# Kernel optimization log

Measured on AMD Instinct MI355X. Metric: run time of the kernel, lower is better.

## Reference

```python
import jax, jax.numpy as jnp
import numpy as np

ALPHA = 4.0   # spikingjelly surrogate.Sigmoid default
TAU = 2.0
VTH = 1.0
EPS = 1e-5

@jax.custom_vjp
def spike(x):
    return (x >= 0.0).astype(x.dtype)

def _spike_fwd(x):
    return spike(x), x

def _spike_bwd(x, g):
    s = jax.nn.sigmoid(ALPHA * x)
    return (g * ALPHA * s * (1.0 - s),)

spike.defvjp(_spike_fwd, _spike_bwd)

def lif(x):
    # x: [T, B, N, C]; multi-step LIF, v_reset=0 hard reset, detach_reset=True
    def step(v, xt):
        v = v + (xt - v) / TAU          # charge
        s = spike(v - VTH)              # fire (surrogate grad)
        v = v * (1.0 - jax.lax.stop_gradient(s))  # hard reset, detached
        return v, s
    _, out = jax.lax.scan(step, jnp.zeros_like(x[0]), x)
    return out

def bn(x, gamma, beta):
    # BatchNorm1d in training mode: per-channel (last dim) over all other dims
    mu = x.mean(axis=(0, 1, 2), keepdims=True)
    var = x.var(axis=(0, 1, 2), keepdims=True)  # biased var, as torch BN uses for normalization
    return (x - mu) * jax.lax.rsqrt(var + EPS) * gamma + beta

def setup_inputs() -> dict:
    key = jax.random.key(0)
    ks = jax.random.split(key, 3)
    T, B, N, C, H = 4, 32, 1024, 256, 256
    x = jax.random.normal(ks[0], (T, B, N, C), dtype=jnp.float32)
    W1 = jax.random.normal(ks[1], (C, H), dtype=jnp.float32) * (1.0 / np.sqrt(C))
    W2 = jax.random.normal(ks[2], (H, C), dtype=jnp.float32) * (1.0 / np.sqrt(H))
    return {
        "x": x,
        "W1": W1, "b1": jnp.zeros((H,), jnp.float32),
        "gamma1": jnp.ones((H,), jnp.float32), "beta1": jnp.zeros((H,), jnp.float32),
        "W2": W2, "b2": jnp.zeros((C,), jnp.float32),
        "gamma2": jnp.ones((C,), jnp.float32), "beta2": jnp.zeros((C,), jnp.float32),
    }

def reference(x, W1, b1, gamma1, beta1, W2, b2, gamma2, beta2):
    # fc1: Linear -> BN (per-channel over T*B*N) -> multi-step LIF
    h = jnp.einsum('tbnc,ch->tbnh', x, W1) + b1
    h = lif(bn(h, gamma1, beta1))
    # fc2
    o = jnp.einsum('tbnh,ho->tbno', h, W2) + b2
    return lif(bn(o, gamma2, beta2))
```

## Files before the change

kernel.cpp:

```cpp
#include <hip/hip_runtime.h>


typedef __attribute__((ext_vector_type(8))) short bf16x8;
typedef __attribute__((ext_vector_type(8))) _Float16 f16x8;
typedef __attribute__((ext_vector_type(4))) _Float16 f16x4;
typedef __attribute__((ext_vector_type(4))) float f32x4;

__device__ __forceinline__ unsigned short f32_to_bf16_rne(float f) {
    unsigned int u = __builtin_bit_cast(unsigned int, f);
    u += 0x7FFFu + ((u >> 16) & 1u);
    return (unsigned short)(u >> 16);
}
__device__ __forceinline__ float bf16_to_f32(unsigned short h) {
    unsigned int u = ((unsigned int)h) << 16;
    return __builtin_bit_cast(float, u);
}
__device__ __forceinline__ int xcd_swz(int bid, int nwg) {
    int per = nwg >> 3;
    return (bid & 7) * per + (bid >> 3);
}

__global__ __launch_bounds__(256) void split_w1(const float* __restrict__ W1,
                                                _Float16* __restrict__ BhiT,
                                                _Float16* __restrict__ BloT) {
    int i = blockIdx.x * 256 + threadIdx.x;
    int k = i >> 8, n = i & 255;
    float w = W1[i];
    _Float16 hi = (_Float16)w;
    _Float16 lo = (_Float16)((w - (float)hi) * 4096.0f);
    BhiT[(size_t)n * 256 + k] = hi;
    BloT[(size_t)n * 256 + k] = lo;
}

__global__ __launch_bounds__(256) void split_w2(const float* __restrict__ W2,
                                                unsigned short* __restrict__ Bt) {
    int i = blockIdx.x * 256 + threadIdx.x;
    int k = i >> 8, n = i & 255;
    float w = W2[i];
    unsigned short hi = f32_to_bf16_rne(w);
    float r = w - bf16_to_f32(hi);
    unsigned short mid = f32_to_bf16_rne(r);
    float r2 = r - bf16_to_f32(mid);
    unsigned short lo = f32_to_bf16_rne(r2);
    Bt[(size_t)(0 * 256 + n) * 256 + k] = hi;
    Bt[(size_t)(1 * 256 + n) * 256 + k] = mid;
    Bt[(size_t)(2 * 256 + n) * 256 + k] = lo;
}

__global__ __launch_bounds__(512, 4) void gemm1_mfma(const float* __restrict__ A,
                                                     const _Float16* __restrict__ Bhi,
                                                     const _Float16* __restrict__ Blo,
                                                     const float* __restrict__ bias,
                                                     float* __restrict__ C,
                                                     double* __restrict__ partial) {
    __shared__ __align__(16) _Float16 Ahi[64 * 256];
    __shared__ __align__(16) _Float16 Alo[64 * 256];
    const int blk = xcd_swz(blockIdx.x, gridDim.x);
    const size_t m0 = (size_t)blk * 64;
    const int tid = threadIdx.x;
    const int lane = tid & 63;
    const int wave = tid >> 6;
    const int lrow = lane & 15, lchunk = lane >> 4;

    const _Float16* BhiB = Bhi + ((size_t)(32 * wave + lrow)) * 256 + lchunk * 8;
    const _Float16* BloB = Blo + ((size_t)(32 * wave + lrow)) * 256 + lchunk * 8;

    {
        const float* src = A + m0 * 256;
        float4 rr[8];
#pragma unroll
        for (int it = 0; it < 8; ++it)
            rr[it] = *(const float4*)(src + (size_t)(it * 512 + tid) * 4);
#pragma unroll
        for (int it = 0; it < 8; ++it) {
            unsigned i4 = (unsigned)(it * 512 + tid);
            float f[4] = {rr[it].x, rr[it].y, rr[it].z, rr[it].w};
            f16x4 hi4, lo4;
#pragma unroll
            for (int e = 0; e < 4; ++e) {
                _Float16 hh = (_Float16)f[e];
                hi4[e] = hh;
                lo4[e] = (_Float16)((f[e] - (float)hh) * 4096.0f);
            }
            unsigned off = i4 * 8u;
            unsigned swz = off ^ (((off >> 9) & 7u) << 4);
            *(f16x4*)((char*)Ahi + swz) = hi4;
            *(f16x4*)((char*)Alo + swz) = lo4;
        }
    }
    __syncthreads();

    f32x4 acc0[4][2] = {}, acc1[4][2] = {};

#pragma unroll
    for (int k0 = 0; k0 < 8; ++k0) {
        f16x8 bh[2], bl[2];
#pragma unroll
        for (int nf = 0; nf < 2; ++nf) {
            bh[nf] = *(const f16x8*)(BhiB + nf * 4096 + k0 * 32);
            bl[nf] = *(const f16x8*)(BloB + nf * 4096 + k0 * 32);
        }
#pragma unroll
        for (int half = 0; half < 2; ++half) {
            f16x8 ah[2], al[2];
#pragma unroll
            for (int m = 0; m < 2; ++m) {
                unsigned r = (unsigned)(32 * half + 16 * m + lrow);
                unsigned off = (r * 512u + (unsigned)(k0 * 64 + lchunk * 16)) ^ ((r & 7u) << 4);
                ah[m] = *(const f16x8*)((const char*)Ahi + off);
                al[m] = *(const f16x8*)((const char*)Alo + off);
            }
            __builtin_amdgcn_s_setprio(1);
#pragma unroll
            for (int nf = 0; nf < 2; ++nf)
#pragma unroll
                for (int m = 0; m < 2; ++m) {
                    const int mf = half * 2 + m;
                    acc0[mf][nf] = __builtin_amdgcn_mfma_f32_16x16x32_f16(
                        ah[m], bh[nf], acc0[mf][nf], 0, 0, 0);
                    acc1[mf][nf] = __builtin_amdgcn_mfma_f32_16x16x32_f16(
                        ah[m], bl[nf], acc1[mf][nf], 0, 0, 0);
                    acc1[mf][nf] = __builtin_amdgcn_mfma_f32_16x16x32_f16(
                        al[m], bh[nf], acc1[mf][nf], 0, 0, 0);
                }
            __builtin_amdgcn_s_setprio(0);
        }
    }

    const float UNSCALE = 1.0f / 4096.0f;
#pragma unroll
    for (int nf = 0; nf < 2; ++nf) {
        int col = 32 * wave + 16 * nf + lrow;
        float bvv = bias[col];
        double ss = 0.0, qq = 0.0;
#pragma unroll
        for (int mf = 0; mf < 4; ++mf) {
            size_t rowb = m0 + 16 * mf + 4 * lchunk;
#pragma unroll
            for (int e = 0; e < 4; ++e) {
                float hv = acc0[mf][nf][e] + acc1[mf][nf][e] * UNSCALE + bvv;
                C[(rowb + e) * 256 + col] = hv;
                ss += (double)hv;
                qq += (double)hv * (double)hv;
            }
        }
        ss += __shfl_xor(ss, 16);
        ss += __shfl_xor(ss, 32);
        qq += __shfl_xor(qq, 16);
        qq += __shfl_xor(qq, 32);
        if (lane < 16) {
            partial[(size_t)blk * 512 + col] = ss;
            partial[(size_t)blk * 512 + 256 + col] = qq;
        }
    }
}

__global__ __launch_bounds__(512, 4) void gemm2_fused(const float* __restrict__ h,
                                                      const float2* __restrict__ ss1,
                                                      const unsigned short* __restrict__ Bt,
                                                      const float* __restrict__ bias,
                                                      float* __restrict__ C,
                                                      double* __restrict__ partial,
                                                      int bnRows) {
    __shared__ __align__(16) unsigned short Asw[64 * 256];
    const int blk = xcd_swz(blockIdx.x, gridDim.x);
    const int bn0 = blk * 16;
    const int tid = threadIdx.x;
    const int lane = tid & 63;
    const int wave = tid >> 6;
    const int lrow = lane & 15, lchunk = lane >> 4;

    const unsigned short* Bbase =
        Bt + ((size_t)(32 * wave + lrow)) * 256 + lchunk * 8;

    {
        float4 rr[8];
#pragma unroll
        for (int it = 0; it < 2; ++it) {
            int slot = it * 512 + tid;
            int bn = slot >> 6;
            int colq = slot & 63;
            size_t rb = (size_t)(bn0 + bn) * 256 + colq * 4;
#pragma unroll
            for (int t4 = 0; t4 < 4; ++t4)
                rr[it * 4 + t4] = *(const float4*)(h + (size_t)t4 * bnRows * 256 + rb);
        }
#pragma unroll
        for (int it = 0; it < 2; ++it) {
            int slot = it * 512 + tid;
            int bn = slot >> 6;
            int colq = slot & 63;
            int c0 = colq * 4;
            float2 p0 = ss1[c0], p1 = ss1[c0 + 1], p2 = ss1[c0 + 2], p3 = ss1[c0 + 3];
            float4 v = make_float4(0.f, 0.f, 0.f, 0.f);
#pragma unroll
            for (int t4 = 0; t4 < 4; ++t4) {
                float4 hv = rr[it * 4 + t4];
                float x0 = hv.x * p0.x + p0.y;
                float x1 = hv.y * p1.x + p1.y;
                float x2 = hv.z * p2.x + p2.y;
                float x3 = hv.w * p3.x + p3.y;
                v.x = (v.x + x0) * 0.5f;
                v.y = (v.y + x1) * 0.5f;
                v.z = (v.z + x2) * 0.5f;
                v.w = (v.w + x3) * 0.5f;
                ushort4 sp;
                sp.x = (v.x >= 1.0f) ? 0x3F80 : 0;
                sp.y = (v.y >= 1.0f) ? 0x3F80 : 0;
                sp.z = (v.z >= 1.0f) ? 0x3F80 : 0;
                sp.w = (v.w >= 1.0f) ? 0x3F80 : 0;
                v.x = (v.x >= 1.0f) ? 0.0f : v.x;
                v.y = (v.y >= 1.0f) ? 0.0f : v.y;
                v.z = (v.z >= 1.0f) ? 0.0f : v.z;
                v.w = (v.w >= 1.0f) ? 0.0f : v.w;
                unsigned row = (unsigned)(t4 * 16 + bn);
                unsigned off = (row * 512u + (unsigned)colq * 8u) ^ ((row & 7u) << 4);
                *(ushort4*)((char*)Asw + off) = sp;
            }
        }
    }
    __syncthreads();

    f32x4 acc[4][2] = {};

#pragma unroll
    for (int k0 = 0; k0 < 8; ++k0) {
        bf16x8 bb[6];
#pragma unroll
        for (int t_ = 0; t_ < 3; ++t_)
#pragma unroll
            for (int nf = 0; nf < 2; ++nf)
                bb[t_ * 2 + nf] = *(const bf16x8*)(Bbase + (size_t)t_ * 65536 +
                                                   nf * 4096 + k0 * 32);
#pragma unroll
        for (int half = 0; half < 2; ++half) {
            bf16x8 af[2];
#pragma unroll
            for (int m = 0; m < 2; ++m) {
                unsigned r = (unsigned)(32 * half + 16 * m + lrow);
                unsigned off = (r * 512u + (unsigned)(k0 * 64 + lchunk * 16)) ^ ((r & 7u) << 4);
                af[m] = *(const bf16x8*)((const char*)Asw + off);
            }
            __builtin_amdgcn_s_setprio(1);
#pragma unroll
            for (int t_ = 0; t_ < 3; ++t_)
#pragma unroll
                for (int nf = 0; nf < 2; ++nf)
#pragma unroll
                    for (int m = 0; m < 2; ++m) {
                        const int mf = half * 2 + m;
                        acc[mf][nf] = __builtin_amdgcn_mfma_f32_16x16x32_bf16(
                            af[m], bb[t_ * 2 + nf], acc[mf][nf], 0, 0, 0);
                    }
            __builtin_amdgcn_s_setprio(0);
        }
    }

#pragma unroll
    for (int nf = 0; nf < 2; ++nf) {
        int col = 32 * wave + 16 * nf + lrow;
        float bvv = bias[col];
        double ss = 0.0, qq = 0.0;
#pragma unroll
        for (int mf = 0; mf < 4; ++mf) {
            int Lbase = 16 * mf + 4 * lchunk;
#pragma unroll
            for (int e = 0; e < 4; ++e) {
                int L = Lbase + e;
                size_t G = (size_t)(L >> 4) * bnRows + bn0 + (L & 15);
                float hv = acc[mf][nf][e] + bvv;
                C[G * 256 + col] = hv;
                ss += (double)hv;
                qq += (double)hv * (double)hv;
            }
        }
        ss += __shfl_xor(ss, 16);
        ss += __shfl_xor(ss, 32);
        qq += __shfl_xor(qq, 16);
        qq += __shfl_xor(qq, 32);
        if (lane < 16) {
            partial[(size_t)blk * 512 + col] = ss;
            partial[(size_t)blk * 512 + 256 + col] = qq;
        }
    }
}

__global__ __launch_bounds__(256) void finalize_stats(const double* __restrict__ partial,
                                                      const float* __restrict__ gamma,
                                                      const float* __restrict__ beta,
                                                      float2* __restrict__ ss,
                                                      int nblocks, double invM) {
    const int c = blockIdx.x;
    const int t = threadIdx.x;
    __shared__ double sh[256];
    __shared__ double sh2[256];
    double s = 0.0, s2 = 0.0;
    for (int b = t; b < nblocks; b += 256) {
        s += partial[(size_t)b * 512 + c];
        s2 += partial[(size_t)b * 512 + 256 + c];
    }
    sh[t] = s;
    sh2[t] = s2;
    __syncthreads();
#pragma unroll
    for (int off = 128; off > 0; off >>= 1) {
        if (t < off) {
            sh[t] += sh[t + off];
            sh2[t] += sh2[t + off];
        }
        __syncthreads();
    }
    if (t == 0) {
        double mu = sh[0] * invM;
        double var = sh2[0] * invM - mu * mu;
        double rstd = 1.0 / sqrt(var + 1e-5);
        double sc = (double)gamma[c] * rstd;
        ss[c] = make_float2((float)sc, (float)((double)beta[c] - mu * sc));
    }
}

__global__ __launch_bounds__(256) void bnlif_f32(const float* __restrict__ h,
                                                 const float2* __restrict__ ss,
                                                 float* __restrict__ out,
                                                 int slab4) {
    int t4 = blockIdx.x * 256 + threadIdx.x;
    if (t4 >= slab4) return;
    size_t idx = (size_t)t4 * 4;
    int c0 = (int)(idx & 255);
    float2 p0 = ss[c0], p1 = ss[c0 + 1], p2 = ss[c0 + 2], p3 = ss[c0 + 3];
    size_t slab = (size_t)slab4 * 4;
    float4 v = make_float4(0.f, 0.f, 0.f, 0.f);
#pragma unroll
    for (int t = 0; t < 4; ++t) {
        float4 hv = *(const float4*)(h + (size_t)t * slab + idx);
        float x0 = hv.x * p0.x + p0.y;
        float x1 = hv.y * p1.x + p1.y;
        float x2 = hv.z * p2.x + p2.y;
        float x3 = hv.w * p3.x + p3.y;
        v.x = (v.x + x0) * 0.5f;
        v.y = (v.y + x1) * 0.5f;
        v.z = (v.z + x2) * 0.5f;
        v.w = (v.w + x3) * 0.5f;
        float4 sp;
        sp.x = (v.x >= 1.0f) ? 1.0f : 0.0f;
        sp.y = (v.y >= 1.0f) ? 1.0f : 0.0f;
        sp.z = (v.z >= 1.0f) ? 1.0f : 0.0f;
        sp.w = (v.w >= 1.0f) ? 1.0f : 0.0f;
        v.x = (v.x >= 1.0f) ? 0.0f : v.x;
        v.y = (v.y >= 1.0f) ? 0.0f : v.y;
        v.z = (v.z >= 1.0f) ? 0.0f : v.z;
        v.w = (v.w >= 1.0f) ? 0.0f : v.w;
        *(float4*)(out + (size_t)t * slab + idx) = sp;
    }
}

extern "C" void kernel_launch(void* const* d_in, const int* in_sizes, int n_in,
                              void* d_out, int out_size, void* d_ws, size_t ws_size,
                              hipStream_t stream) {
    const float* x  = (const float*)d_in[0];
    const float* W1 = (const float*)d_in[1];
    const float* b1 = (const float*)d_in[2];
    const float* g1 = (const float*)d_in[3];
    const float* be1 = (const float*)d_in[4];
    const float* W2 = (const float*)d_in[5];
    const float* b2 = (const float*)d_in[6];
    const float* g2 = (const float*)d_in[7];
    const float* be2 = (const float*)d_in[8];
    float* out = (float*)d_out;

    const int M = in_sizes[0] / 256;
    const int bnRows = M / 4;
    const size_t hBytes = (size_t)M * 256 * 4;

    char* ws = (char*)d_ws;
    float* h = (float*)ws;
    double* partial = (double*)(ws + hBytes);
    unsigned short* W2catT = (unsigned short*)(ws + hBytes + (size_t)2048 * 512 * 8);
    float2* ss1 = (float2*)((char*)W2catT + 3 * 256 * 256 * 2);
    float2* ss2 = ss1 + 256;
    _Float16* W1hiT = (_Float16*)(ss2 + 256);
    _Float16* W1loT = W1hiT + 256 * 256;

    const int slab4 = M * 16;
    const double invM = 1.0 / (double)M;
    const int NB1 = M / 64;
    const int NB2 = bnRows / 16;

    dim3 blk(256);

    split_w1<<<dim3(256), blk, 0, stream>>>(W1, W1hiT, W1loT);
    split_w2<<<dim3(256), blk, 0, stream>>>(W2, W2catT);

    gemm1_mfma<<<dim3(NB1), dim3(512), 0, stream>>>(x, W1hiT, W1loT, b1, h, partial);
    finalize_stats<<<dim3(256), blk, 0, stream>>>(partial, g1, be1, ss1, NB1, invM);

    gemm2_fused<<<dim3(NB2), dim3(512), 0, stream>>>(h, ss1, W2catT, b2, h, partial, bnRows);
    finalize_stats<<<dim3(256), blk, 0, stream>>>(partial, g2, be2, ss2, NB2, invM);
    bnlif_f32<<<dim3(slab4 / 256), blk, 0, stream>>>(h, ss2, out, slab4);
}
```

Baseline: 290.7 us.

## Split K into two halves and overlap second-half loads with first-half MFMA

Result: slower. 321.0 us (+10.4%).

```diff
diff --git a/kernel.cpp b/kernel.cpp
--- a/kernel.cpp
+++ b/kernel.cpp
@@ -53,8 +53,8 @@
                                                      const float* __restrict__ bias,
                                                      float* __restrict__ C,
                                                      double* __restrict__ partial) {
-    __shared__ __align__(16) _Float16 Ahi[64 * 256];
-    __shared__ __align__(16) _Float16 Alo[64 * 256];
+    __shared__ __align__(16) _Float16 AhiS[2][64 * 128];
+    __shared__ __align__(16) _Float16 AloS[2][64 * 128];
     const int blk = xcd_swz(blockIdx.x, gridDim.x);
     const size_t m0 = (size_t)blk * 64;
     const int tid = threadIdx.x;
@@ -65,67 +65,75 @@
     const _Float16* BhiB = Bhi + ((size_t)(32 * wave + lrow)) * 256 + lchunk * 8;
     const _Float16* BloB = Blo + ((size_t)(32 * wave + lrow)) * 256 + lchunk * 8;
 
-    {
-        const float* src = A + m0 * 256;
-        float4 rr[8];
-#pragma unroll
-        for (int it = 0; it < 8; ++it)
-            rr[it] = *(const float4*)(src + (size_t)(it * 512 + tid) * 4);
-#pragma unroll
-        for (int it = 0; it < 8; ++it) {
-            unsigned i4 = (unsigned)(it * 512 + tid);
-            float f[4] = {rr[it].x, rr[it].y, rr[it].z, rr[it].w};
-            f16x4 hi4, lo4;
-#pragma unroll
-            for (int e = 0; e < 4; ++e) {
-                _Float16 hh = (_Float16)f[e];
-                hi4[e] = hh;
-                lo4[e] = (_Float16)((f[e] - (float)hh) * 4096.0f);
-            }
-            unsigned off = i4 * 8u;
-            unsigned swz = off ^ (((off >> 9) & 7u) << 4);
-            *(f16x4*)((char*)Ahi + swz) = hi4;
-            *(f16x4*)((char*)Alo + swz) = lo4;
-        }
-    }
+    float4 ra[4], rb[4];
+#define ISSUE1(R, ck)                                                         \
+    {                                                                         \
+        const float* s_ = A + m0 * 256 + (ck) * 128;                          \
+        _Pragma("unroll") for (int j = 0; j < 4; ++j) {                       \
+            unsigned i4 = (unsigned)(j * 512 + tid);                          \
+            R[j] = *(const float4*)(s_ + (size_t)(i4 >> 5) * 256 + (i4 & 31) * 4); \
+        }                                                                     \
+    }
+#define CW1(R, buf)                                                           \
+    _Pragma("unroll") for (int j = 0; j < 4; ++j) {                           \
+        unsigned i4 = (unsigned)(j * 512 + tid);                              \
+        unsigned row = i4 >> 5, colq = i4 & 31;                               \
+        float f0 = R[j].x, f1 = R[j].y, f2 = R[j].z, f3 = R[j].w;             \
+        f16x4 hi4, lo4;                                                       \
+        _Float16 h0 = (_Float16)f0; hi4[0] = h0; lo4[0] = (_Float16)((f0 - (float)h0) * 4096.0f); \
+        _Float16 h1 = (_Float16)f1; hi4[1] = h1; lo4[1] = (_Float16)((f1 - (float)h1) * 4096.0f); \
+        _Float16 h2 = (_Float16)f2; hi4[2] = h2; lo4[2] = (_Float16)((f2 - (float)h2) * 4096.0f); \
+        _Float16 h3 = (_Float16)f3; hi4[3] = h3; lo4[3] = (_Float16)((f3 - (float)h3) * 4096.0f); \
+        unsigned off = (row * 256u + colq * 8u) ^ ((row & 7u) << 4);          \
+        *(f16x4*)((char*)AhiS[buf] + off) = hi4;                              \
+        *(f16x4*)((char*)AloS[buf] + off) = lo4;                              \
+    }
+
+    ISSUE1(ra, 0)
+    CW1(ra, 0)
+    ISSUE1(rb, 1)
     __syncthreads();
 
     f32x4 acc0[4][2] = {}, acc1[4][2] = {};
 
-#pragma unroll
-    for (int k0 = 0; k0 < 8; ++k0) {
-        f16x8 bh[2], bl[2];
-#pragma unroll
-        for (int nf = 0; nf < 2; ++nf) {
-            bh[nf] = *(const f16x8*)(BhiB + nf * 4096 + k0 * 32);
-            bl[nf] = *(const f16x8*)(BloB + nf * 4096 + k0 * 32);
-        }
-#pragma unroll
-        for (int half = 0; half < 2; ++half) {
-            f16x8 ah[2], al[2];
-#pragma unroll
-            for (int m = 0; m < 2; ++m) {
-                unsigned r = (unsigned)(32 * half + 16 * m + lrow);
-                unsigned off = (r * 512u + (unsigned)(k0 * 64 + lchunk * 16)) ^ ((r & 7u) << 4);
-                ah[m] = *(const f16x8*)((const char*)Ahi + off);
-                al[m] = *(const f16x8*)((const char*)Alo + off);
-            }
-            __builtin_amdgcn_s_setprio(1);
-#pragma unroll
-            for (int nf = 0; nf < 2; ++nf)
-#pragma unroll
-                for (int m = 0; m < 2; ++m) {
-                    const int mf = half * 2 + m;
-                    acc0[mf][nf] = __builtin_amdgcn_mfma_f32_16x16x32_f16(
-                        ah[m], bh[nf], acc0[mf][nf], 0, 0, 0);
-                    acc1[mf][nf] = __builtin_amdgcn_mfma_f32_16x16x32_f16(
-                        ah[m], bl[nf], acc1[mf][nf], 0, 0, 0);
-                    acc1[mf][nf] = __builtin_amdgcn_mfma_f32_16x16x32_f16(
-                        al[m], bh[nf], acc1[mf][nf], 0, 0, 0);
-                }
-            __builtin_amdgcn_s_setprio(0);
-        }
-    }
+#define COMPUTE1(buf, K0)                                                     \
+    _Pragma("unroll") for (int kl = 0; kl < 4; ++kl) {                        \
+        const int k0 = (K0) + kl;                                             \
+        f16x8 bh[2], bl[2];                                                   \
+        _Pragma("unroll") for (int nf = 0; nf < 2; ++nf) {                    \
+            bh[nf] = *(const f16x8*)(BhiB + nf * 4096 + k0 * 32);             \
+            bl[nf] = *(const f16x8*)(BloB + nf * 4096 + k0 * 32);             \
+        }                                                                     \
+        _Pragma("unroll") for (int half = 0; half < 2; ++half) {              \
+            f16x8 ah[2], al[2];                                               \
+            _Pragma("unroll") for (int m = 0; m < 2; ++m) {                   \
+                unsigned r = (unsigned)(32 * half + 16 * m + lrow);           \
+                unsigned off = (r * 256u + (unsigned)(kl * 64 + lchunk * 16)) ^ ((r & 7u) << 4); \
+                ah[m] = *(const f16x8*)((const char*)AhiS[buf] + off);        \
+                al[m] = *(const f16x8*)((const char*)AloS[buf] + off);        \
+            }                                                                 \
+            __builtin_amdgcn_s_setprio(1);                                    \
+            _Pragma("unroll") for (int nf = 0; nf < 2; ++nf)                  \
+            _Pragma("unroll") for (int m = 0; m < 2; ++m) {                   \
+                const int mf = half * 2 + m;                                  \
+                acc0[mf][nf] = __builtin_amdgcn_mfma_f32_16x16x32_f16(        \
+                    ah[m], bh[nf], acc0[mf][nf], 0, 0, 0);                    \
+                acc1[mf][nf] = __builtin_amdgcn_mfma_f32_16x16x32_f16(        \
+                    ah[m], bl[nf], acc1[mf][nf], 0, 0, 0);                    \
+                acc1[mf][nf] = __builtin_amdgcn_mfma_f32_16x16x32_f16(        \
+                    al[m], bh[nf], acc1[mf][nf], 0, 0, 0);                    \
+            }                                                                 \
+            __builtin_amdgcn_s_setprio(0);                                    \
+        }                                                                     \
+    }
+
+    COMPUTE1(0, 0)
+    CW1(rb, 1)
+    __syncthreads();
+    COMPUTE1(1, 4)
+#undef ISSUE1
+#undef CW1
+#undef COMPUTE1
 
     const float UNSCALE = 1.0f / 4096.0f;
 #pragma unroll
@@ -162,7 +170,7 @@
                                                       float* __restrict__ C,
                                                       double* __restrict__ partial,
                                                       int bnRows) {
-    __shared__ __align__(16) unsigned short Asw[64 * 256];
+    __shared__ __align__(16) unsigned short AswS[2][64 * 128];
     const int blk = xcd_swz(blockIdx.x, gridDim.x);
     const int bn0 = blk * 16;
     const int tid = threadIdx.x;
@@ -173,88 +181,85 @@
     const unsigned short* Bbase =
         Bt + ((size_t)(32 * wave + lrow)) * 256 + lchunk * 8;
 
-    {
-        float4 rr[8];
-#pragma unroll
-        for (int it = 0; it < 2; ++it) {
-            int slot = it * 512 + tid;
-            int bn = slot >> 6;
-            int colq = slot & 63;
-            size_t rb = (size_t)(bn0 + bn) * 256 + colq * 4;
-#pragma unroll
-            for (int t4 = 0; t4 < 4; ++t4)
-                rr[it * 4 + t4] = *(const float4*)(h + (size_t)t4 * bnRows * 256 + rb);
-        }
-#pragma unroll
-        for (int it = 0; it < 2; ++it) {
-            int slot = it * 512 + tid;
-            int bn = slot >> 6;
-            int colq = slot & 63;
-            int c0 = colq * 4;
-            float2 p0 = ss1[c0], p1 = ss1[c0 + 1], p2 = ss1[c0 + 2], p3 = ss1[c0 + 3];
-            float4 v = make_float4(0.f, 0.f, 0.f, 0.f);
-#pragma unroll
-            for (int t4 = 0; t4 < 4; ++t4) {
-                float4 hv = rr[it * 4 + t4];
-                float x0 = hv.x * p0.x + p0.y;
-                float x1 = hv.y * p1.x + p1.y;
-                float x2 = hv.z * p2.x + p2.y;
-                float x3 = hv.w * p3.x + p3.y;
-                v.x = (v.x + x0) * 0.5f;
-                v.y = (v.y + x1) * 0.5f;
-                v.z = (v.z + x2) * 0.5f;
-                v.w = (v.w + x3) * 0.5f;
-                ushort4 sp;
-                sp.x = (v.x >= 1.0f) ? 0x3F80 : 0;
-                sp.y = (v.y >= 1.0f) ? 0x3F80 : 0;
-                sp.z = (v.z >= 1.0f) ? 0x3F80 : 0;
-                sp.w = (v.w >= 1.0f) ? 0x3F80 : 0;
-                v.x = (v.x >= 1.0f) ? 0.0f : v.x;
-                v.y = (v.y >= 1.0f) ? 0.0f : v.y;
-                v.z = (v.z >= 1.0f) ? 0.0f : v.z;
-                v.w = (v.w >= 1.0f) ? 0.0f : v.w;
-                unsigned row = (unsigned)(t4 * 16 + bn);
-                unsigned off = (row * 512u + (unsigned)colq * 8u) ^ ((row & 7u) << 4);
-                *(ushort4*)((char*)Asw + off) = sp;
-            }
-        }
-    }
+    const int sbn = tid >> 5, scq = tid & 31;
+    float4 ra[4], rb[4];
+#define ISSUE2(R, ck)                                                         \
+    {                                                                         \
+        size_t rb_ = (size_t)(bn0 + sbn) * 256 + (ck) * 128 + scq * 4;        \
+        _Pragma("unroll") for (int t4 = 0; t4 < 4; ++t4)                      \
+            R[t4] = *(const float4*)(h + (size_t)t4 * bnRows * 256 + rb_);    \
+    }
+#define CW2(R, buf, ck)                                                       \
+    {                                                                         \
+        int c0 = (ck) * 128 + scq * 4;                                        \
+        float2 p0 = ss1[c0], p1 = ss1[c0 + 1], p2 = ss1[c0 + 2], p3 = ss1[c0 + 3]; \
+        float4 v = make_float4(0.f, 0.f, 0.f, 0.f);                           \
+        _Pragma("unroll") for (int t4 = 0; t4 < 4; ++t4) {                    \
+            float4 hv = R[t4];                                                \
+            float x0 = hv.x * p0.x + p0.y;                                    \
+            float x1 = hv.y * p1.x + p1.y;                                    \
+            float x2 = hv.z * p2.x + p2.y;                                    \
+            float x3 = hv.w * p3.x + p3.y;                                    \
+            v.x = (v.x + x0) * 0.5f;                                          \
+            v.y = (v.y + x1) * 0.5f;                                          \
+            v.z = (v.z + x2) * 0.5f;                                          \
+            v.w = (v.w + x3) * 0.5f;                                          \
+            ushort4 sp;                                                       \
+            sp.x = (v.x >= 1.0f) ? 0x3F80 : 0;                                \
+            sp.y = (v.y >= 1.0f) ? 0x3F80 : 0;                                \
+            sp.z = (v.z >= 1.0f) ? 0x3F80 : 0;                                \
+            sp.w = (v.w >= 1.0f) ? 0x3F80 : 0;                                \
+            v.x = (v.x >= 1.0f) ? 0.0f : v.x;                                 \
+            v.y = (v.y >= 1.0f) ? 0.0f : v.y;                                 \
+            v.z = (v.z >= 1.0f) ? 0.0f : v.z;                                 \
+            v.w = (v.w >= 1.0f) ? 0.0f : v.w;                                 \
+            unsigned row = (unsigned)(t4 * 16 + sbn);                         \
+            unsigned off = (row * 256u + (unsigned)scq * 8u) ^ ((row & 7u) << 4); \
+            *(ushort4*)((char*)AswS[buf] + off) = sp;                         \
+        }                                                                     \
+    }
+
+    ISSUE2(ra, 0)
+    CW2(ra, 0, 0)
+    ISSUE2(rb, 1)
     __syncthreads();
 
     f32x4 acc[4][2] = {};
 
-#pragma unroll
-    for (int k0 = 0; k0 < 8; ++k0) {
-        bf16x8 bb[6];
-#pragma unroll
-        for (int t_ = 0; t_ < 3; ++t_)
-#pragma unroll
-            for (int nf = 0; nf < 2; ++nf)
-                bb[t_ * 2 + nf] = *(const bf16x8*)(Bbase + (size_t)t_ * 65536 +
-                                                   nf * 4096 + k0 * 32);
-#pragma unroll
-        for (int half = 0; half < 2; ++half) {
-            bf16x8 af[2];
-#pragma unroll
-            for (int m = 0; m < 2; ++m) {
-                unsigned r = (unsigned)(32 * half + 16 * m + lrow);
-                unsigned off = (r * 512u + (unsigned)(k0 * 64 + lchunk * 16)) ^ ((r & 7u) << 4);
-                af[m] = *(const bf16x8*)((const char*)Asw + off);
-            }
-            __builtin_amdgcn_s_setprio(1);
-#pragma unroll
-            for (int t_ = 0; t_ < 3; ++t_)
-#pragma unroll
-                for (int nf = 0; nf < 2; ++nf)
-#pragma unroll
-                    for (int m = 0; m < 2; ++m) {
-                        const int mf = half * 2 + m;
-                        acc[mf][nf] = __builtin_amdgcn_mfma_f32_16x16x32_bf16(
-                            af[m], bb[t_ * 2 + nf], acc[mf][nf], 0, 0, 0);
-                    }
-            __builtin_amdgcn_s_setprio(0);
-        }
-    }
+#define COMPUTE2(buf, K0)                                                     \
+    _Pragma("unroll") for (int kl = 0; kl < 4; ++kl) {                        \
+        const int k0 = (K0) + kl;                                             \
+        bf16x8 bb[6];                                                         \
+        _Pragma("unroll") for (int t_ = 0; t_ < 3; ++t_)                      \
+        _Pragma("unroll") for (int nf = 0; nf < 2; ++nf)                      \
+            bb[t_ * 2 + nf] = *(const bf16x8*)(Bbase + (size_t)t_ * 65536 +   \
+                                               nf * 4096 + k0 * 32);          \
+        _Pragma("unroll") for (int half = 0; half < 2; ++half) {              \
+            bf16x8 af[2];                                                     \
+            _Pragma("unroll") for (int m = 0; m < 2; ++m) {                   \
+                unsigned r = (unsigned)(32 * half + 16 * m + lrow);           \
+                unsigned off = (r * 256u + (unsigned)(kl * 64 + lchunk * 16)) ^ ((r & 7u) << 4); \
+                af[m] = *(const bf16x8*)((const char*)AswS[buf] + off);       \
+            }                                                                 \
+            __builtin_amdgcn_s_setprio(1);                                    \
+            _Pragma("unroll") for (int t_ = 0; t_ < 3; ++t_)                  \
+            _Pragma("unroll") for (int nf = 0; nf < 2; ++nf)                  \
+            _Pragma("unroll") for (int m = 0; m < 2; ++m) {                   \
+                const int mf = half * 2 + m;                                  \
+                acc[mf][nf] = __builtin_amdgcn_mfma_f32_16x16x32_bf16(        \
+                    af[m], bb[t_ * 2 + nf], acc[mf][nf], 0, 0, 0);            \
+            }                                                                 \
+            __builtin_amdgcn_s_setprio(0);                                    \
+        }                                                                     \
+    }
+
+    COMPUTE2(0, 0)
+    CW2(rb, 1, 1)
+    __syncthreads();
+    COMPUTE2(1, 4)
+#undef ISSUE2
+#undef CW2
+#undef COMPUTE2
 
 #pragma unroll
     for (int nf = 0; nf < 2; ++nf) {
```
